# Optimization experiments

Measured on AMD Instinct MI355X. Metric: run time of the kernel, lower is better.

## Reference

```python
import jax, jax.numpy as jnp
import numpy as np

HEADS = 8
RANK = 4

def _lora(x, w_down, w_up, palette, in_dim, out_dim):
    # w_down: [RANK*in_dim, 15], w_up: [RANK*out_dim, 15], palette: [1, 15]
    down = (palette @ w_down.T).reshape(RANK, in_dim)   # [r, in]
    up = (palette @ w_up.T).reshape(out_dim, RANK)      # [out, r]
    return (x @ down.T) @ up.T                          # [..., out]


def setup_inputs() -> dict:
    key = jax.random.key(0)
    ks = jax.random.split(key, 16)
    B, S, D = 2, 2048, 1280
    def n(k, shape, std=0.02):
        return (jax.random.normal(k, shape, dtype=jnp.float32) * std).astype(jnp.float32)
    return {
        'hidden_states': jax.random.normal(ks[0], (B, S, D), dtype=jnp.float32),
        'color_palette': jax.random.uniform(ks[1], (1, 15), dtype=jnp.float32),
        'Wq': n(ks[2], (D, D)), 'Wk': n(ks[3], (D, D)),
        'Wv': n(ks[4], (D, D)), 'Wo': n(ks[5], (D, D)),
        'bo': jnp.zeros((D,), dtype=jnp.float32),
        'q_down': n(ks[6], (RANK * D, 15), 0.25), 'q_up': n(ks[7], (RANK * D, 15)),
        'k_down': n(ks[8], (RANK * D, 15), 0.25), 'k_up': n(ks[9], (RANK * D, 15)),
        'v_down': n(ks[10], (RANK * D, 15), 0.25), 'v_up': n(ks[11], (RANK * D, 15)),
        'o_down': n(ks[12], (RANK * D, 15), 0.25), 'o_up': n(ks[13], (RANK * D, 15)),
    }


def reference(hidden_states, color_palette, Wq, Wk, Wv, Wo, bo,
              q_down, q_up, k_down, k_up, v_down, v_up, o_down, o_up):
    B, S, D = hidden_states.shape
    H = HEADS
    hd = D // H
    scale = 1.0  # LoRA scale
    x = hidden_states
    # LoRA-augmented projections (self-attention: encoder_hidden_states = x)
    q = x @ Wq.T + scale * _lora(x, q_down, q_up, color_palette, D, D)
    k = x @ Wk.T + scale * _lora(x, k_down, k_up, color_palette, D, D)
    v = x @ Wv.T + scale * _lora(x, v_down, v_up, color_palette, D, D)
    # split heads: [B, S, D] -> [B, H, S, hd]
    q = q.reshape(B, S, H, hd).transpose(0, 2, 1, 3)
    k = k.reshape(B, S, H, hd).transpose(0, 2, 1, 3)
    v = v.reshape(B, S, H, hd).transpose(0, 2, 1, 3)
    attn_scale = 1.0 / jnp.sqrt(jnp.asarray(hd, dtype=q.dtype))
    scores = jnp.einsum('bhqd,bhkd->bhqk', q, k) * attn_scale
    probs = jax.nn.softmax(scores, axis=-1)
    out = jnp.einsum('bhqk,bhkd->bhqd', probs, v)
    out = out.transpose(0, 2, 1, 3).reshape(B, S, D)
    out = out @ Wo.T + bo + scale * _lora(out, o_down, o_up, color_palette, D, D)
    return out
```

## Files before the change

kernel.cpp:

```cpp
#include <hip/hip_runtime.h>

typedef unsigned short u16;
typedef unsigned int u32;
typedef __attribute__((ext_vector_type(4))) float floatx4;
typedef __attribute__((ext_vector_type(16))) float floatx16;
typedef __attribute__((ext_vector_type(8))) __bf16 bf16x8;

#define MFMA_BF16(a, b, c) __builtin_amdgcn_mfma_f32_16x16x32_bf16((a), (b), (c), 0, 0, 0)
#define MFMA32(a, b, c) __builtin_amdgcn_mfma_f32_32x32x16_bf16((a), (b), (c), 0, 0, 0)

typedef const __attribute__((address_space(1))) void* gas_ptr;
typedef __attribute__((address_space(3))) void* las_ptr;

__device__ __forceinline__ void gll16(const void* g, void* l) {
  __builtin_amdgcn_global_load_lds((gas_ptr)g, (las_ptr)l, 16, 0, 0);
}

__device__ __forceinline__ u16 f2bf(float x) {
  u32 u = __builtin_bit_cast(u32, x);
  u = (u + 0x7fffu + ((u >> 16) & 1u)) >> 16;
  return (u16)u;
}

__global__ void prep_downup(const float* __restrict__ pal,
                            const float* __restrict__ qd, const float* __restrict__ qu,
                            const float* __restrict__ kd, const float* __restrict__ ku,
                            const float* __restrict__ vd, const float* __restrict__ vu,
                            const float* __restrict__ od, const float* __restrict__ ou,
                            float* __restrict__ down_f, float* __restrict__ up_f) {
  int tid = blockIdx.x * blockDim.x + threadIdx.x;
  int w = tid / 10240;
  int rem = tid - w * 10240;
  const float* dsrc = (w == 0) ? qd : (w == 1) ? kd : (w == 2) ? vd : od;
  const float* usrc = (w == 0) ? qu : (w == 1) ? ku : (w == 2) ? vu : ou;
  bool isdown = rem < 5120;
  int row = isdown ? rem : rem - 5120;
  const float* src = (isdown ? dsrc : usrc) + row * 15;
  float s = 0.f;
#pragma unroll
  for (int p = 0; p < 15; ++p) s += pal[p] * src[p];
  if (isdown) down_f[w * 5120 + row] = s;
  else        up_f[w * 5120 + row] = s;
}

__global__ void build_weff(const float* __restrict__ Wq, const float* __restrict__ Wk,
                           const float* __restrict__ Wv, const float* __restrict__ Wo,
                           const float* __restrict__ down_f, const float* __restrict__ up_f,
                           u16* __restrict__ weff_qkv, u16* __restrict__ weff_o) {
  int tid = blockIdx.x * blockDim.x + threadIdx.x;
  int w = tid / 1638400;
  int rem = tid - w * 1638400;
  int n = rem / 1280;
  int k = rem - n * 1280;
  const float* W = (w == 0) ? Wq : (w == 1) ? Wk : (w == 2) ? Wv : Wo;
  const float* up = up_f + w * 5120 + n * 4;
  const float* dn = down_f + w * 5120 + k;
  float v = W[rem] + up[0] * dn[0] + up[1] * dn[1280] + up[2] * dn[2560] + up[3] * dn[3840];
  u16 hv = f2bf(v);
  if (w < 3) weff_qkv[w * 1638400 + rem] = hv;
  else       weff_o[rem] = hv;
}

__global__ void cvt_x(const float4* __restrict__ x, ushort4* __restrict__ xb) {
  int i = blockIdx.x * blockDim.x + threadIdx.x;
  float4 v = x[i];
  ushort4 o;
  o.x = f2bf(v.x); o.y = f2bf(v.y); o.z = f2bf(v.z); o.w = f2bf(v.w);
  xb[i] = o;
}

__global__ __launch_bounds__(256) void gemm128_qkv(const u16* __restrict__ A, const u16* __restrict__ Bm,
                                                   u16* __restrict__ qb, u16* __restrict__ kb,
                                                   u16* __restrict__ vbuf, int K) {
  __shared__ __align__(16) u16 lA[128 * 64];
  __shared__ __align__(16) u16 lB[128 * 64];
  const int t = threadIdx.x;
  const int lane = t & 63;
  const int l15 = lane & 15, quad = lane >> 4;
  const int wid = t >> 6;
  const int wm = (wid >> 1) * 64;
  const int wn = (wid & 1) * 64;
  const int bm = blockIdx.x * 128;
  const int bn = blockIdx.y * 128;
  floatx4 acc[4][4] = {};

  int soff[4];
#pragma unroll
  for (int i = 0; i < 4; ++i) {
    int c = t + i * 256;
    int row = c >> 3, pos = c & 7;
    soff[i] = row * K + ((pos + row) & 7) * 8;
  }
  int afo[4][2], bfo[4][2];
#pragma unroll
  for (int i = 0; i < 4; ++i) {
#pragma unroll
    for (int ch = 0; ch < 2; ++ch) {
      int ra = wm + i * 16 + l15;
      int rb = wn + i * 16 + l15;
      int kc8 = ch * 4 + quad;
      afo[i][ch] = ra * 64 + ((kc8 - ra) & 7) * 8;
      bfo[i][ch] = rb * 64 + ((kc8 - rb) & 7) * 8;
    }
  }

  const u16* Ab = A + (long)bm * K;
  const u16* Bb = Bm + (long)bn * K;
  const int nkt = K >> 6;

  for (int kt = 0; kt < nkt; ++kt) {
    __syncthreads();
    const int k0 = kt * 64;
#pragma unroll
    for (int i = 0; i < 4; ++i) gll16(Ab + (long)soff[i] + k0, lA + (t + i * 256) * 8);
#pragma unroll
    for (int i = 0; i < 4; ++i) gll16(Bb + (long)soff[i] + k0, lB + (t + i * 256) * 8);
    __syncthreads();
#pragma unroll
    for (int ch = 0; ch < 2; ++ch) {
      bf16x8 af[4], bfr[4];
#pragma unroll
      for (int i = 0; i < 4; ++i) af[i] = *(const bf16x8*)(lA + afo[i][ch]);
#pragma unroll
      for (int i = 0; i < 4; ++i) bfr[i] = *(const bf16x8*)(lB + bfo[i][ch]);
#pragma unroll
      for (int i = 0; i < 4; ++i)
#pragma unroll
        for (int j = 0; j < 4; ++j)
          acc[i][j] = MFMA_BF16(af[i], bfr[j], acc[i][j]);
    }
  }

#pragma unroll
  for (int i = 0; i < 4; ++i) {
#pragma unroll
    for (int j = 0; j < 4; ++j) {
#pragma unroll
      for (int r = 0; r < 4; ++r) {
        int m = bm + wm + i * 16 + quad * 4 + r;
        int n = bn + wn + j * 16 + l15;
        u16 hv = f2bf(acc[i][j][r]);
        if (n < 1280) {
          qb[(long)m * 1280 + n] = hv;
        } else if (n < 2560) {
          kb[(long)m * 1280 + (n - 1280)] = hv;
        } else {
          vbuf[(long)m * 1280 + (n - 2560)] = hv;
        }
      }
    }
  }
}

__global__ __launch_bounds__(256) void vtrans(const u16* __restrict__ vbuf,
                                              u16* __restrict__ vtb) {
  __shared__ u16 tile[64 * 65];
  const int t = threadIdx.x;
  const int sb = blockIdx.x * 64, nb = blockIdx.y * 64, b = blockIdx.z;
  const u16* src = vbuf + ((long)(b * 2048 + sb)) * 1280 + nb;
#pragma unroll
  for (int it = 0; it < 16; ++it) {
    int idx = t + it * 256;
    int s = idx >> 6, n = idx & 63;
    tile[s * 65 + n] = src[(long)s * 1280 + n];
  }
  __syncthreads();
  u16* dst = vtb + ((long)(b * 1280 + nb)) * 2048 + sb;
#pragma unroll
  for (int it = 0; it < 16; ++it) {
    int idx = t + it * 256;
    int n = idx >> 6, s = idx & 63;
    dst[(long)n * 2048 + s] = tile[s * 65 + n];
  }
}

__global__ __launch_bounds__(256) void gemm64_o(const u16* __restrict__ A, const u16* __restrict__ Bm,
                                                float* __restrict__ outf,
                                                const float* __restrict__ bias, int K) {
  __shared__ __align__(16) u16 lA[64 * 64];
  __shared__ __align__(16) u16 lB[128 * 64];
  const int t = threadIdx.x;
  const int lane = t & 63;
  const int l15 = lane & 15, quad = lane >> 4;
  const int wid = t >> 6;
  const int bm = blockIdx.x * 64;
  const int bn = blockIdx.y * 128;
  floatx4 acc[4][2] = {};

  int aoff[2], boff[4];
#pragma unroll
  for (int i = 0; i < 2; ++i) {
    int c = t + i * 256;
    int row = c >> 3, pos = c & 7;
    aoff[i] = row * K + ((pos + row) & 7) * 8;
  }
#pragma unroll
  for (int i = 0; i < 4; ++i) {
    int c = t + i * 256;
    int row = c >> 3, pos = c & 7;
    boff[i] = row * K + ((pos + row) & 7) * 8;
  }
  int afo[4][2], bfo[2][2];
#pragma unroll
  for (int ch = 0; ch < 2; ++ch) {
    int kc8 = ch * 4 + quad;
#pragma unroll
    for (int i = 0; i < 4; ++i) {
      int ra = i * 16 + l15;
      afo[i][ch] = ra * 64 + ((kc8 - ra) & 7) * 8;
    }
#pragma unroll
    for (int j = 0; j < 2; ++j) {
      int rb = wid * 32 + j * 16 + l15;
      bfo[j][ch] = rb * 64 + ((kc8 - rb) & 7) * 8;
    }
  }

  const u16* Ab = A + (long)bm * K;
  const u16* Bb = Bm + (long)bn * K;
  const int nkt = K >> 6;

  for (int kt = 0; kt < nkt; ++kt) {
    __syncthreads();
    const int k0 = kt * 64;
#pragma unroll
    for (int i = 0; i < 2; ++i) gll16(Ab + (long)aoff[i] + k0, lA + (t + i * 256) * 8);
#pragma unroll
    for (int i = 0; i < 4; ++i) gll16(Bb + (long)boff[i] + k0, lB + (t + i * 256) * 8);
    __syncthreads();
#pragma unroll
    for (int ch = 0; ch < 2; ++ch) {
      bf16x8 af[4], bfr[2];
#pragma unroll
      for (int i = 0; i < 4; ++i) af[i] = *(const bf16x8*)(lA + afo[i][ch]);
#pragma unroll
      for (int j = 0; j < 2; ++j) bfr[j] = *(const bf16x8*)(lB + bfo[j][ch]);
#pragma unroll
      for (int i = 0; i < 4; ++i)
#pragma unroll
        for (int j = 0; j < 2; ++j)
          acc[i][j] = MFMA_BF16(af[i], bfr[j], acc[i][j]);
    }
  }

#pragma unroll
  for (int i = 0; i < 4; ++i) {
#pragma unroll
    for (int j = 0; j < 2; ++j) {
#pragma unroll
      for (int r = 0; r < 4; ++r) {
        int m = bm + i * 16 + quad * 4 + r;
        int n = bn + wid * 32 + j * 16 + l15;
        outf[(long)m * 1280 + n] = acc[i][j][r] + bias[n];
      }
    }
  }
}

__global__ __launch_bounds__(512) void flash_attn(const u16* __restrict__ qb,
                                                  const u16* __restrict__ kb,
                                                  const u16* __restrict__ vtb,
                                                  u16* __restrict__ attn) {
  const int D = 1280, HD = 160;
  __shared__ __align__(16) u16 kv_lds[2][20480];
  __shared__ __align__(16) u16 p_lds[8][1024];
  const int t = threadIdx.x, lane = t & 63, wid = t >> 6;
  const int l31 = lane & 31, hi = lane >> 5;
  const int rg = wid >> 1, kh = wid & 1;
  const int bh = blockIdx.y, b = bh >> 3, h = bh & 7;
  const int q0 = blockIdx.x * 128 + rg * 32;
  const float kS = 0.11404582025f;

  bf16x8 aq[10];
  {
    const u16* qg = qb + ((long)(b * 2048 + q0 + l31)) * D + h * HD + hi * 8;
#pragma unroll
    for (int kw = 0; kw < 10; ++kw) aq[kw] = *(const bf16x8*)(qg + kw * 16);
  }

  const u16* sg[5];
  int sadv[5];
#pragma unroll
  for (int i = 0; i < 5; ++i) {
    int c = t + i * 512;
    if (c < 1280) {
      int key = c / 20, pos = c - key * 20;
      int ccol = pos - (key % 20);
      if (ccol < 0) ccol += 20;
      sg[i] = kb + ((long)(b * 2048 + key)) * D + h * HD + ccol * 8;
      sadv[i] = 64 * D;
    } else {
      int c2 = c - 1280;
      int vrow = c2 >> 3, swz = c2 & 7;
      int vcol = swz ^ (vrow & 7);
      sg[i] = vtb + ((long)(b * 1280 + h * HD + vrow)) * 2048 + vcol * 8;
      sadv[i] = 64;
    }
  }

  int kfo[10];
  {
    int key = kh * 32 + l31;
#pragma unroll
    for (int kw = 0; kw < 10; ++kw) {
      int g = kw * 2 + hi;
      int pos = (g + key) % 20;
      kfo[kw] = (key * 20 + pos) * 8;
    }
  }
  int vfo[5][2];
#pragma unroll
  for (int db = 0; db < 5; ++db) {
#pragma unroll
    for (int kwv = 0; kwv < 2; ++kwv) {
      int d = db * 32 + l31;
      int gc = kh * 4 + kwv * 2 + hi;
      int sw = gc ^ (d & 7);
      vfo[db][kwv] = 10240 + (d * 8 + sw) * 8;
    }
  }
  int pfo[2];
#pragma unroll
  for (int ks = 0; ks < 2; ++ks)
    pfo[ks] = l31 * 64 + (((ks * 2 + hi) ^ (l31 & 3)) << 4);

  float l_acc[16] = {};
  floatx16 o_acc[5] = {};

#pragma unroll
  for (int i = 0; i < 5; ++i) {
    gll16(sg[i], &kv_lds[0][0] + (t + i * 512) * 8);
    sg[i] += sadv[i];
  }

  for (int kt0 = 0; kt0 < 32; ++kt0) {
    u16* cbase = &kv_lds[kt0 & 1][0];
    if (kt0 < 31) {
      u16* nbase = &kv_lds[(kt0 & 1) ^ 1][0];
#pragma unroll
      for (int i = 0; i < 5; ++i) {
        gll16(sg[i], nbase + (t + i * 512) * 8);
        sg[i] += sadv[i];
      }
      asm volatile("s_waitcnt vmcnt(5)" ::: "memory");
    } else {
      asm volatile("s_waitcnt vmcnt(0)" ::: "memory");
    }
    __builtin_amdgcn_s_barrier();
    __builtin_amdgcn_sched_barrier(0);

    floatx16 s0 = {}, s1 = {};
#pragma unroll
    for (int kw = 0; kw < 5; ++kw) {
      bf16x8 k0 = *(const bf16x8*)(cbase + kfo[kw * 2]);
      bf16x8 k1 = *(const bf16x8*)(cbase + kfo[kw * 2 + 1]);
      s0 = MFMA32(aq[kw * 2], k0, s0);
      s1 = MFMA32(aq[kw * 2 + 1], k1, s1);
    }

    u16* pw = p_lds[wid];
#pragma unroll
    for (int r = 0; r < 16; ++r) {
      float sv = (s0[r] + s1[r]) * kS;
      float p = __builtin_exp2f(fminf(sv, 80.f));
      l_acc[r] += p;
      int qr = (r & 3) + 8 * (r >> 2) + 4 * hi;
      int boff = qr * 64 + (((l31 >> 3) ^ (r & 3)) << 4) + (l31 & 7) * 2;
      *(u16*)((char*)pw + boff) = f2bf(p);
    }
    asm volatile("s_waitcnt lgkmcnt(0)" ::: "memory");
    __builtin_amdgcn_sched_barrier(0);

    bf16x8 pa0 = *(const bf16x8*)((const char*)pw + pfo[0]);
    bf16x8 pa1 = *(const bf16x8*)((const char*)pw + pfo[1]);
#pragma unroll
    for (int db = 0; db < 5; ++db) {
      bf16x8 v0 = *(const bf16x8*)(cbase + vfo[db][0]);
      bf16x8 v1 = *(const bf16x8*)(cbase + vfo[db][1]);
      o_acc[db] = MFMA32(pa0, v0, o_acc[db]);
      o_acc[db] = MFMA32(pa1, v1, o_acc[db]);
    }
    __builtin_amdgcn_sched_barrier(0);
    __builtin_amdgcn_s_barrier();
  }

  float* oscr = (float*)&kv_lds[0][0];
  float* lscr = (float*)&p_lds[0][0];
  if (kh == 1) {
#pragma unroll
    for (int db = 0; db < 5; ++db)
#pragma unroll
      for (int r = 0; r < 16; ++r)
        oscr[rg * 5120 + (db * 16 + r) * 64 + lane] = o_acc[db][r];
#pragma unroll
    for (int r = 0; r < 16; ++r)
      lscr[rg * 1024 + r * 64 + lane] = l_acc[r];
  }
  __syncthreads();
  if (kh == 0) {
    float rl[16];
#pragma unroll
    for (int r = 0; r < 16; ++r) {
      float rs = l_acc[r] + lscr[rg * 1024 + r * 64 + lane];
      rs += __shfl_xor(rs, 1, 64);
      rs += __shfl_xor(rs, 2, 64);
      rs += __shfl_xor(rs, 4, 64);
      rs += __shfl_xor(rs, 8, 64);
      rs += __shfl_xor(rs, 16, 64);
      rl[r] = 1.0f / rs;
    }
#pragma unroll
    for (int db = 0; db < 5; ++db) {
#pragma unroll
      for (int r = 0; r < 16; ++r) {
        float v = (o_acc[db][r] + oscr[rg * 5120 + (db * 16 + r) * 64 + lane]) * rl[r];
        int row = q0 + (r & 3) + 8 * (r >> 2) + 4 * hi;
        int col = h * HD + db * 32 + l31;
        attn[((long)(b * 2048 + row)) * D + col] = f2bf(v);
      }
    }
  }
}

extern "C" void kernel_launch(void* const* d_in, const int* in_sizes, int n_in,
                              void* d_out, int out_size, void* d_ws, size_t ws_size,
                              hipStream_t stream) {
  const float* x   = (const float*)d_in[0];
  const float* pal = (const float*)d_in[1];
  const float* Wq  = (const float*)d_in[2];
  const float* Wk  = (const float*)d_in[3];
  const float* Wv  = (const float*)d_in[4];
  const float* Wo  = (const float*)d_in[5];
  const float* bo  = (const float*)d_in[6];
  const float* qd  = (const float*)d_in[7];
  const float* qu  = (const float*)d_in[8];
  const float* kd  = (const float*)d_in[9];
  const float* ku  = (const float*)d_in[10];
  const float* vd  = (const float*)d_in[11];
  const float* vu  = (const float*)d_in[12];
  const float* od  = (const float*)d_in[13];
  const float* ou  = (const float*)d_in[14];
  float* out = (float*)d_out;

  char* ws = (char*)d_ws;
  u16* xb       = (u16*)(ws);
  u16* weff_qkv = (u16*)(ws + 10485760);
  u16* weff_o   = (u16*)(ws + 20316160);
  u16* qbuf     = (u16*)(ws + 23592960);
  u16* kbuf     = (u16*)(ws + 34078720);
  u16* vtb      = (u16*)(ws + 44564480);
  u16* attn     = (u16*)(ws + 55050240);
  float* down_f = (float*)(ws + 65536000);
  float* up_f   = (float*)(ws + 65617920);
  u16* vbuf     = (u16*)(ws + 65699840);

  prep_downup<<<160, 256, 0, stream>>>(pal, qd, qu, kd, ku, vd, vu, od, ou, down_f, up_f);
  build_weff<<<25600, 256, 0, stream>>>(Wq, Wk, Wv, Wo, down_f, up_f, weff_qkv, weff_o);
  cvt_x<<<5120, 256, 0, stream>>>((const float4*)x, (ushort4*)xb);
  gemm128_qkv<<<dim3(32, 30), 256, 0, stream>>>(xb, weff_qkv, qbuf, kbuf, vbuf, 1280);
  vtrans<<<dim3(32, 20, 2), 256, 0, stream>>>(vbuf, vtb);
  flash_attn<<<dim3(16, 16), 512, 0, stream>>>(qbuf, kbuf, vtb, attn);
  gemm64_o<<<dim3(64, 10), 256, 0, stream>>>(attn, weff_o, out, bo, 1280);
}
```

Baseline: 284.6 us.

## Compute transposed scores to keep P in registers via permlane32 swap

Swaps MFMA operand order so the score tile comes out transposed (keys along rows, queries per lane). P can then be packed with v_cvt_pk_bf16_f32 and redistributed with permlane32_swap directly into the PV MFMA A-operand, with no round trip through shared memory. This removes the P LDS scratch buffer, its stores, the lgkmcnt wait and the reloads. It also merges the two partial-sum score accumulators into one dependent MFMA chain of 10, which lengthens latency, and restructures the row-sum reduction to a per-lane scalar combined through LDS at the end.

```diff
diff --git a/kernel.cpp b/kernel.cpp
--- a/kernel.cpp
+++ b/kernel.cpp
@@ -5,6 +5,8 @@
 typedef __attribute__((ext_vector_type(4))) float floatx4;
 typedef __attribute__((ext_vector_type(16))) float floatx16;
 typedef __attribute__((ext_vector_type(8))) __bf16 bf16x8;
+typedef __attribute__((ext_vector_type(2))) unsigned int u32x2;
+typedef __attribute__((ext_vector_type(4))) unsigned int u32x4;
 
 #define MFMA_BF16(a, b, c) __builtin_amdgcn_mfma_f32_16x16x32_bf16((a), (b), (c), 0, 0, 0)
 #define MFMA32(a, b, c) __builtin_amdgcn_mfma_f32_32x32x16_bf16((a), (b), (c), 0, 0, 0)
@@ -20,6 +22,12 @@
   u32 u = __builtin_bit_cast(u32, x);
   u = (u + 0x7fffu + ((u >> 16) & 1u)) >> 16;
   return (u16)u;
+}
+
+__device__ __forceinline__ u32 cvtpk(float lo, float hi) {
+  u32 r;
+  asm("v_cvt_pk_bf16_f32 %0, %1, %2" : "=v"(r) : "v"(lo), "v"(hi));
+  return r;
 }
 
 __global__ void prep_downup(const float* __restrict__ pal,
@@ -263,7 +271,6 @@
                                                   u16* __restrict__ attn) {
   const int D = 1280, HD = 160;
   __shared__ __align__(16) u16 kv_lds[2][20480];
-  __shared__ __align__(16) u16 p_lds[8][1024];
   const int t = threadIdx.x, lane = t & 63, wid = t >> 6;
   const int l31 = lane & 31, hi = lane >> 5;
   const int rg = wid >> 1, kh = wid & 1;
@@ -312,19 +319,15 @@
 #pragma unroll
   for (int db = 0; db < 5; ++db) {
 #pragma unroll
-    for (int kwv = 0; kwv < 2; ++kwv) {
+    for (int w = 0; w < 2; ++w) {
       int d = db * 32 + l31;
-      int gc = kh * 4 + kwv * 2 + hi;
+      int gc = kh * 4 + w * 2 + hi;
       int sw = gc ^ (d & 7);
-      vfo[db][kwv] = 10240 + (d * 8 + sw) * 8;
-    }
-  }
-  int pfo[2];
-#pragma unroll
-  for (int ks = 0; ks < 2; ++ks)
-    pfo[ks] = l31 * 64 + (((ks * 2 + hi) ^ (l31 & 3)) << 4);
-
-  float l_acc[16] = {};
+      vfo[db][w] = 10240 + (d * 8 + sw) * 8;
+    }
+  }
+
+  float l_sum = 0.f;
   floatx16 o_acc[5] = {};
 
 #pragma unroll
@@ -349,30 +352,34 @@
     __builtin_amdgcn_s_barrier();
     __builtin_amdgcn_sched_barrier(0);
 
-    floatx16 s0 = {}, s1 = {};
-#pragma unroll
-    for (int kw = 0; kw < 5; ++kw) {
-      bf16x8 k0 = *(const bf16x8*)(cbase + kfo[kw * 2]);
-      bf16x8 k1 = *(const bf16x8*)(cbase + kfo[kw * 2 + 1]);
-      s0 = MFMA32(aq[kw * 2], k0, s0);
-      s1 = MFMA32(aq[kw * 2 + 1], k1, s1);
-    }
-
-    u16* pw = p_lds[wid];
+    floatx16 s = {};
+#pragma unroll
+    for (int kw = 0; kw < 10; ++kw) {
+      bf16x8 kf = *(const bf16x8*)(cbase + kfo[kw]);
+      s = MFMA32(kf, aq[kw], s);
+    }
+
+    float p[16];
 #pragma unroll
     for (int r = 0; r < 16; ++r) {
-      float sv = (s0[r] + s1[r]) * kS;
-      float p = __builtin_exp2f(fminf(sv, 80.f));
-      l_acc[r] += p;
-      int qr = (r & 3) + 8 * (r >> 2) + 4 * hi;
-      int boff = qr * 64 + (((l31 >> 3) ^ (r & 3)) << 4) + (l31 & 7) * 2;
-      *(u16*)((char*)pw + boff) = f2bf(p);
-    }
-    asm volatile("s_waitcnt lgkmcnt(0)" ::: "memory");
-    __builtin_amdgcn_sched_barrier(0);
-
-    bf16x8 pa0 = *(const bf16x8*)((const char*)pw + pfo[0]);
-    bf16x8 pa1 = *(const bf16x8*)((const char*)pw + pfo[1]);
+      p[r] = __builtin_exp2f(fminf(s[r] * kS, 80.f));
+      l_sum += p[r];
+    }
+
+    u32 c01 = cvtpk(p[0], p[1]),  c23 = cvtpk(p[2], p[3]);
+    u32 c45 = cvtpk(p[4], p[5]),  c67 = cvtpk(p[6], p[7]);
+    u32 c89 = cvtpk(p[8], p[9]),  cAB = cvtpk(p[10], p[11]);
+    u32 cCD = cvtpk(p[12], p[13]), cEF = cvtpk(p[14], p[15]);
+
+    u32x2 r02 = __builtin_amdgcn_permlane32_swap(c01, c45, false, false);
+    u32x2 r13 = __builtin_amdgcn_permlane32_swap(c23, c67, false, false);
+    u32x2 r46 = __builtin_amdgcn_permlane32_swap(c89, cCD, false, false);
+    u32x2 r57 = __builtin_amdgcn_permlane32_swap(cAB, cEF, false, false);
+    u32x4 pk0 = {r02[0], r13[0], r02[1], r13[1]};
+    u32x4 pk1 = {r46[0], r57[0], r46[1], r57[1]};
+    bf16x8 pa0 = __builtin_bit_cast(bf16x8, pk0);
+    bf16x8 pa1 = __builtin_bit_cast(bf16x8, pk1);
+
 #pragma unroll
     for (int db = 0; db < 5; ++db) {
       bf16x8 v0 = *(const bf16x8*)(cbase + vfo[db][0]);
@@ -384,31 +391,28 @@
     __builtin_amdgcn_s_barrier();
   }
 
+  float* lscr = (float*)&kv_lds[0][0];
+  lscr[wid * 64 + lane] = l_sum;
+  __syncthreads();
+  float rl[16];
+#pragma unroll
+  for (int r = 0; r < 16; ++r) {
+    int q32 = (r & 3) + 8 * (r >> 2) + 4 * hi;
+    float tot = lscr[(rg * 2 + 0) * 64 + q32] + lscr[(rg * 2 + 0) * 64 + q32 + 32]
+              + lscr[(rg * 2 + 1) * 64 + q32] + lscr[(rg * 2 + 1) * 64 + q32 + 32];
+    rl[r] = 1.0f / tot;
+  }
+  __syncthreads();
   float* oscr = (float*)&kv_lds[0][0];
-  float* lscr = (float*)&p_lds[0][0];
   if (kh == 1) {
 #pragma unroll
     for (int db = 0; db < 5; ++db)
 #pragma unroll
       for (int r = 0; r < 16; ++r)
         oscr[rg * 5120 + (db * 16 + r) * 64 + lane] = o_acc[db][r];
-#pragma unroll
-    for (int r = 0; r < 16; ++r)
-      lscr[rg * 1024 + r * 64 + lane] = l_acc[r];
   }
   __syncthreads();
   if (kh == 0) {
-    float rl[16];
-#pragma unroll
-    for (int r = 0; r < 16; ++r) {
-      float rs = l_acc[r] + lscr[rg * 1024 + r * 64 + lane];
-      rs += __shfl_xor(rs, 1, 64);
-      rs += __shfl_xor(rs, 2, 64);
-      rs += __shfl_xor(rs, 4, 64);
-      rs += __shfl_xor(rs, 8, 64);
-      rs += __shfl_xor(rs, 16, 64);
-      rl[r] = 1.0f / rs;
-    }
 #pragma unroll
     for (int db = 0; db < 5; ++db) {
 #pragma unroll
```

After: 269.3 us. 5.4% less time.
